# Optimization experiments

Hardware: AMD Instinct MI355X
Metric: run time of the kernel (lower is better)

## Reference

```python
import jax, jax.numpy as jnp
import numpy as np

D = 2048      # d_model
H = 16        # n_heads
M = 8         # n_modalities (== seq_len, forced by attn_mask shape)
S = 8         # seq_len per modality
E = 8         # num_experts
K = 3         # top_k
SPARSITY = 0.1


def setup_inputs() -> dict:
    key = jax.random.key(0)
    ks = jax.random.split(key, 24)
    w = lambda i, shape, s=0.02: (jax.random.normal(ks[i], shape, jnp.float32) * s)
    return {
        'feats': jax.random.normal(ks[0], (M, S, D), jnp.float32),
        'context': jax.random.normal(ks[1], (D,), jnp.float32),
        'mod_emb': jax.random.normal(ks[2], (M, D), jnp.float32),  # torch.randn
        'rW1': w(3, (D, 2 * D)), 'rb1': jnp.zeros((D,), jnp.float32),
        'rW2': w(4, (D // 2, D)), 'rb2': jnp.zeros((D // 2,), jnp.float32),
        'rW3': w(5, (1, D // 2)), 'rb3': jnp.zeros((1,), jnp.float32),
        'W_in': w(6, (3 * D, D)), 'b_in': jnp.zeros((3 * D,), jnp.float32),
        'W_out': w(7, (D, D)), 'b_out': jnp.zeros((D,), jnp.float32),
        'gW1': w(8, (D // 2, D)), 'gb1': jnp.zeros((D // 2,), jnp.float32),
        'gW2': w(9, (E, D // 2)), 'gb2': jnp.zeros((E,), jnp.float32),
        'eW1': w(10, (E, 2 * D, D)), 'eb1': jnp.zeros((E, 2 * D), jnp.float32),
        'eW2': w(11, (E, D, 2 * D)), 'eb2': jnp.zeros((E, D), jnp.float32),
        'e_gamma': jnp.ones((E, D), jnp.float32),
        'e_beta': jnp.zeros((E, D), jnp.float32),
    }


def reference(feats, context, mod_emb, rW1, rb1, rW2, rb2, rW3, rb3,
              W_in, b_in, W_out, b_out, gW1, gb1, gW2, gb2,
              eW1, eb1, eW2, eb2, e_gamma, e_beta):
    # --- modality embedding enhancement ---
    x = feats + mod_emb[:, None, :]                                # [M,S,D]

    # --- dynamic modality routing ---
    summ = x.mean(axis=1)                                          # [M,D] (mean over seq dim 0 of each 2D feat)
    comb = jnp.concatenate([summ, jnp.broadcast_to(context, summ.shape)], axis=-1)  # [M,2D]
    h = jax.nn.relu(comb @ rW1.T + rb1)
    h = jax.nn.relu(h @ rW2.T + rb2)
    rw = jax.nn.sigmoid(h @ rW3.T + rb3)[:, 0]                     # [M]
    rw = rw / rw.sum()                                             # sigmoid>0 so total>0 branch

    # --- sparse attention mask from routing weights ---
    wmat = rw[:, None] * rw[None, :]                               # [M,M]
    thr = jnp.quantile(wmat.reshape(-1), 1.0 - SPARSITY)
    mask = jnp.where(wmat < thr, jnp.float32(-1e9), jnp.float32(0.0))  # [M,M] == [S,S]

    # --- multi-head self-attention (batch=M modalities, seq=S, eval mode) ---
    qkv = x @ W_in.T + b_in                                        # [M,S,3D]
    q, k, v = jnp.split(qkv, 3, axis=-1)
    hd = D // H
    q = q.reshape(M, S, H, hd); k = k.reshape(M, S, H, hd); v = v.reshape(M, S, H, hd)
    scores = jnp.einsum('bqhd,bkhd->bhqk', q, k) / np.sqrt(hd)     # [M,H,S,S]
    scores = scores + mask                                         # broadcast [S,S] additive mask
    attn = jax.nn.softmax(scores, axis=-1)
    o = jnp.einsum('bhqk,bkhd->bqhd', attn, v).reshape(M, S, D)
    o = o @ W_out.T + b_out                                        # [M,S,D]

    # attended.mean(dim=0).squeeze() then view(-1)[:D] == first row of the mean
    attended = o.mean(axis=0)[0]                                   # [D]

    # --- mixture-of-experts fusion on the single token ---
    g = jax.nn.relu(attended @ gW1.T + gb1)
    gate_probs = jax.nn.softmax(g @ gW2.T + gb2)                   # [E]
    top_v, top_i = jax.lax.top_k(gate_probs, K)
    gates = jax.nn.softmax(top_v)                                  # renormalized top-k gates
    W1k, b1k = eW1[top_i], eb1[top_i]                              # [K,2D,D],[K,2D]
    W2k, b2k = eW2[top_i], eb2[top_i]                              # [K,D,2D],[K,D]
    gk, bk = e_gamma[top_i], e_beta[top_i]                         # [K,D]
    hh = jax.nn.gelu(jnp.einsum('d,kod->ko', attended, W1k) + b1k, approximate=False)
    y = jnp.einsum('ko,kdo->kd', hh, W2k) + b2k                    # [K,D]
    mu = y.mean(axis=-1, keepdims=True)
    var = ((y - mu) ** 2).mean(axis=-1, keepdims=True)
    ln = (y - mu) / jnp.sqrt(var + 1e-5) * gk + bk                 # per-expert LayerNorm
    fused = (gates[:, None] * ln).sum(axis=0)                      # [D]
    return fused, rw
```

## Files before the change

### kernel.cpp

```cpp
#include <hip/hip_runtime.h>
#include <math.h>

namespace {

constexpr int Dm = 2048;

using f4n = __attribute__((ext_vector_type(4))) float;

__device__ __forceinline__ float dot4(float4 u, float4 v) {
  return u.x * v.x + u.y * v.y + u.z * v.z + u.w * v.w;
}
__device__ __forceinline__ float4 add4(float4 u, float4 v) {
  return make_float4(u.x + v.x, u.y + v.y, u.z + v.z, u.w + v.w);
}
__device__ __forceinline__ float dot4nt(const float* p, float4 a) {
  f4n w = __builtin_nontemporal_load((const f4n*)p);
  return w.x * a.x + w.y * a.y + w.z * a.z + w.w * a.w;
}

__device__ __forceinline__ void top3_from_logits(const float* l, int* ti) {
  int used0 = -1, used1 = -1;
  for (int kk = 0; kk < 3; ++kk) {
    float bv = -1e30f; int bi = -1;
#pragma unroll
    for (int e = 0; e < 8; ++e) {
      if (e == used0 || e == used1) continue;
      if (l[e] > bv) { bv = l[e]; bi = e; }
    }
    ti[kk] = bi;
    if (kk == 0) used0 = bi; else if (kk == 1) used1 = bi;
  }
}

__global__ __launch_bounds__(256) void k_summ(const float* __restrict__ feats,
                                              const float* __restrict__ mod,
                                              float* __restrict__ summ,
                                              float* __restrict__ msum,
                                              float* __restrict__ logits) {
  int t4 = blockIdx.x * 256 + threadIdx.x;
  int elem = t4 * 4;
  int m = elem >> 11;
  float4 s = make_float4(0.f, 0.f, 0.f, 0.f);
#pragma unroll
  for (int t = 0; t < 8; ++t)
    s = add4(s, *(const float4*)(feats + ((size_t)(m * 8 + t) << 11) + (elem & 2047)));
  float4 md = *(const float4*)(mod + elem);
  *(float4*)(summ + elem) = make_float4(s.x * 0.125f + md.x, s.y * 0.125f + md.y,
                                        s.z * 0.125f + md.z, s.w * 0.125f + md.w);
  if (t4 < 512) {
    int i4 = t4 * 4;
    float4 acc = make_float4(0.f, 0.f, 0.f, 0.f);
#pragma unroll
    for (int mm = 0; mm < 8; ++mm)
      acc = add4(acc, *(const float4*)(mod + ((size_t)mm << 11) + i4));
    *(float4*)(msum + i4) = acc;
  }
  if (blockIdx.x == 0 && threadIdx.x < 8) logits[threadIdx.x] = 0.f;
}

__global__ __launch_bounds__(256) void k_big1(const float* __restrict__ summ,
                                              const float* __restrict__ ctx,
                                              const float* __restrict__ feats,
                                              const float* __restrict__ mod,
                                              const float* __restrict__ rW1,
                                              const float* __restrict__ rb1,
                                              const float* __restrict__ W_in,
                                              const float* __restrict__ b_in,
                                              float* __restrict__ h1,
                                              float* __restrict__ q0) {
  __shared__ float As[8 * Dm];
  int tid = threadIdx.x, wave = tid >> 6, lane = tid & 63;
  if (blockIdx.x < 512) {
    for (int t = tid; t < 8 * Dm; t += 256) As[t] = summ[t];
    __syncthreads();
    int j = blockIdx.x * 4 + wave;
    const float* Wr = rW1 + (size_t)j * 4096;
    float acc[8] = {0, 0, 0, 0, 0, 0, 0, 0};
    float accC = 0.f;
    for (int i = lane * 4; i < Dm; i += 256) {
      float4 w1 = *(const float4*)(Wr + i);
      float4 w2 = *(const float4*)(Wr + 2048 + i);
      float4 c = *(const float4*)(ctx + i);
      accC += dot4(w2, c);
#pragma unroll
      for (int m = 0; m < 8; ++m) {
        float4 a = *(const float4*)(As + (m << 11) + i);
        acc[m] += dot4(w1, a);
      }
    }
#pragma unroll
    for (int o = 32; o > 0; o >>= 1) {
      accC += __shfl_down(accC, o, 64);
#pragma unroll
      for (int m = 0; m < 8; ++m) acc[m] += __shfl_down(acc[m], o, 64);
    }
    if (lane == 0) {
      float base = accC + rb1[j];
#pragma unroll
      for (int m = 0; m < 8; ++m) h1[(m << 11) + j] = fmaxf(acc[m] + base, 0.f);
    }
  } else {
    for (int t = tid; t < 8 * Dm; t += 256) {
      int m = t >> 11, col = t & 2047;
      As[t] = feats[(size_t)(m * 8) * Dm + col] + mod[(m << 11) + col];
    }
    __syncthreads();
    int j = (blockIdx.x - 512) * 4 + wave;
    const float* Wr = W_in + (size_t)j * Dm;
    float acc[8] = {0, 0, 0, 0, 0, 0, 0, 0};
    for (int i = lane * 4; i < Dm; i += 256) {
      float4 w = *(const float4*)(Wr + i);
#pragma unroll
      for (int m = 0; m < 8; ++m) {
        float4 a = *(const float4*)(As + (m << 11) + i);
        acc[m] += dot4(w, a);
      }
    }
#pragma unroll
    for (int o = 32; o > 0; o >>= 1)
#pragma unroll
      for (int m = 0; m < 8; ++m) acc[m] += __shfl_down(acc[m], o, 64);
    if (lane == 0) {
      float b = b_in[j];
#pragma unroll
      for (int m = 0; m < 8; ++m) q0[(m << 11) + j] = acc[m] + b;
    }
  }
}

__global__ __launch_bounds__(256) void k_big2(const float* __restrict__ h1,
                                              const float* __restrict__ rW2,
                                              const float* __restrict__ rb2,
                                              const float* __restrict__ q0,
                                              const float* __restrict__ W_in,
                                              float* __restrict__ h2,
                                              float* __restrict__ qw) {
  __shared__ float As[8 * Dm];
  int tid = threadIdx.x, wave = tid >> 6, lane = tid & 63;
  if (blockIdx.x < 256) {
    for (int t = tid; t < 8 * Dm; t += 256) As[t] = h1[t];
    __syncthreads();
    int j = blockIdx.x * 4 + wave;
    const float* Wr = rW2 + (size_t)j * Dm;
    float acc[8] = {0, 0, 0, 0, 0, 0, 0, 0};
    for (int i = lane * 4; i < Dm; i += 256) {
      float4 w = *(const float4*)(Wr + i);
#pragma unroll
      for (int m = 0; m < 8; ++m) {
        float4 a = *(const float4*)(As + (m << 11) + i);
        acc[m] += dot4(w, a);
      }
    }
#pragma unroll
    for (int o = 32; o > 0; o >>= 1)
#pragma unroll
      for (int m = 0; m < 8; ++m) acc[m] += __shfl_down(acc[m], o, 64);
    if (lane == 0) {
      float b = rb2[j];
#pragma unroll
      for (int m = 0; m < 8; ++m) h2[m * 1024 + j] = fmaxf(acc[m] + b, 0.f);
    }
  } else {
    int bb = blockIdx.x - 256;
    int h = bb >> 3, chunk = bb & 7;
    int c0 = chunk * 256;
    float* qs = As;
    float* red = As + 1024;
    for (int t = tid; t < 1024; t += 256) {
      int m = t >> 7, d = t & 127;
      qs[t] = q0[(m << 11) + h * 128 + d];
    }
    __syncthreads();
    float4 acc[8];
#pragma unroll
    for (int m = 0; m < 8; ++m) acc[m] = make_float4(0.f, 0.f, 0.f, 0.f);
    const float* Wb = W_in + (size_t)(Dm + h * 128 + wave * 32) * Dm + c0 + lane * 4;
#pragma unroll 8
    for (int d = 0; d < 32; ++d) {
      float4 wv = *(const float4*)(Wb + (size_t)d * Dm);
#pragma unroll
      for (int m = 0; m < 8; ++m) {
        float q = qs[(m << 7) + wave * 32 + d];
        acc[m].x += wv.x * q; acc[m].y += wv.y * q;
        acc[m].z += wv.z * q; acc[m].w += wv.w * q;
      }
    }
#pragma unroll
    for (int m = 0; m < 8; ++m)
      *(float4*)(red + (((wave << 3) + m) << 8) + lane * 4) = acc[m];
    __syncthreads();
    int m = tid >> 5, c = (tid & 31) * 8;
    float4 s0 = make_float4(0.f, 0.f, 0.f, 0.f);
    float4 s1 = make_float4(0.f, 0.f, 0.f, 0.f);
#pragma unroll
    for (int w = 0; w < 4; ++w) {
      s0 = add4(s0, *(const float4*)(red + (((w << 3) + m) << 8) + c));
      s1 = add4(s1, *(const float4*)(red + (((w << 3) + m) << 8) + c + 4));
    }
    float* dst = qw + (size_t)(m * 16 + h) * Dm + c0 + c;
    *(float4*)dst = s0;
    *(float4*)(dst + 4) = s1;
  }
}

__global__ __launch_bounds__(256) void k_attnw(const float* __restrict__ h2,
                                               const float* __restrict__ rW3,
                                               const float* __restrict__ rb3,
                                               const float* __restrict__ qw,
                                               const float* __restrict__ feats,
                                               float* __restrict__ att,
                                               float* __restrict__ out_rw) {
  __shared__ float sig[8], wm[64], sv[64], mask_s[8];
  int tid = threadIdx.x, wave = tid >> 6, lane = tid & 63;
  for (int mi = 0; mi < 2; ++mi) {
    int m = wave + mi * 4;
    float acc = 0.f;
    for (int i = lane * 4; i < 1024; i += 256) {
      float4 w = *(const float4*)(rW3 + i);
      float4 a = *(const float4*)(h2 + m * 1024 + i);
      acc += dot4(w, a);
    }
#pragma unroll
    for (int o = 32; o > 0; o >>= 1) acc += __shfl_down(acc, o, 64);
    if (lane == 0) sig[m] = 1.f / (1.f + expf(-(acc + rb3[0])));
  }
  __syncthreads();
  if (tid < 64) {
    float tot = 0.f;
#pragma unroll
    for (int m = 0; m < 8; ++m) tot += sig[m];
    int r = tid >> 3, cc = tid & 7;
    wm[tid] = (sig[r] / tot) * (sig[cc] / tot);
    if (blockIdx.x == 0 && tid < 8) out_rw[tid] = sig[tid] / tot;
  }
  __syncthreads();
  if (tid < 64) {
    float v = wm[tid];
    int rank = 0;
    for (int t = 0; t < 64; ++t) {
      float u = wm[t];
      rank += (u < v) || (u == v && t < tid);
    }
    sv[rank] = v;
  }
  __syncthreads();
  if (tid < 8) {
    double pos = 0.9 * 63.0;
    int lo = (int)pos;
    double frac = pos - (double)lo;
    float thr = (float)((double)sv[lo] + frac * ((double)sv[lo + 1] - (double)sv[lo]));
    mask_s[tid] = (wm[tid] < thr) ? -1e9f : 0.f;
  }
  __syncthreads();
  {
    int mh = blockIdx.x * 4 + wave;
    int m = mh >> 4;
    const float* qr = qw + (size_t)mh * Dm;
    float sc[8];
#pragma unroll
    for (int k = 0; k < 8; ++k) {
      const float* fr = feats + (size_t)(m * 8 + k) * Dm;
      float acc = 0.f;
#pragma unroll
      for (int i = 0; i < 8; ++i) {
        int idx = lane * 4 + i * 256;
        acc += dot4(*(const float4*)(qr + idx), *(const float4*)(fr + idx));
      }
#pragma unroll
      for (int o = 32; o > 0; o >>= 1) acc += __shfl_xor(acc, o, 64);
      sc[k] = acc * 0.08838834764831845f + mask_s[k];
    }
    float mx = sc[0];
#pragma unroll
    for (int k = 1; k < 8; ++k) mx = fmaxf(mx, sc[k]);
    float se = 0.f;
#pragma unroll
    for (int k = 0; k < 8; ++k) { sc[k] = expf(sc[k] - mx); se += sc[k]; }
    float inv = 1.f / se;
    if (lane == 0) {
#pragma unroll
      for (int k = 0; k < 8; ++k) att[mh * 8 + k] = sc[k] * inv;
    }
  }
}

__global__ __launch_bounds__(256) void k_xbar(const float* __restrict__ att,
                                              const float* __restrict__ feats,
                                              const float* __restrict__ msum,
                                              float* __restrict__ xbar) {
  __shared__ float aw[64];
  int h = blockIdx.y;
  int i = blockIdx.x * 256 + threadIdx.x;
  if (threadIdx.x < 64) {
    int m = threadIdx.x >> 3, k = threadIdx.x & 7;
    aw[threadIdx.x] = att[(m * 16 + h) * 8 + k];
  }
  __syncthreads();
  float acc = msum[i];
#pragma unroll
  for (int b = 0; b < 64; ++b) acc += aw[b] * feats[(size_t)b * Dm + i];
  xbar[(size_t)h * Dm + i] = acc * 0.125f;
}

template <int ACT>
__global__ __launch_bounds__(256) void k_matvec8(const float* __restrict__ A, int G,
                                                 const float* __restrict__ W,
                                                 const float* __restrict__ b1,
                                                 float* __restrict__ out) {
  int j0 = blockIdx.x * 8;
  const float* Arow = A + (size_t)(j0 / G) * Dm;
  int wave = threadIdx.x >> 6, lane = threadIdx.x & 63;
  int j = j0 + wave * 2;
  const float* W0 = W + (size_t)j * Dm;
  const float* W1 = W0 + Dm;
  float acc0 = 0.f, acc1 = 0.f;
#pragma unroll 8
  for (int i = lane * 4; i < Dm; i += 256) {
    float4 a = *(const float4*)(Arow + i);
    acc0 += dot4(*(const float4*)(W0 + i), a);
    acc1 += dot4(*(const float4*)(W1 + i), a);
  }
#pragma unroll
  for (int o = 32; o > 0; o >>= 1) {
    acc0 += __shfl_down(acc0, o, 64);
    acc1 += __shfl_down(acc1, o, 64);
  }
  if (lane == 0) {
    float v0 = acc0 + b1[j], v1 = acc1 + b1[j + 1];
    if (ACT == 1) { v0 = fmaxf(v0, 0.f); v1 = fmaxf(v1, 0.f); }
    out[j] = v0;
    out[j + 1] = v1;
  }
}

__global__ __launch_bounds__(256) void k_gbufL(const float* __restrict__ attd,
                                               const float* __restrict__ gW1,
                                               const float* __restrict__ gb1,
                                               const float* __restrict__ gW2,
                                               float* __restrict__ logits) {
  __shared__ float gv[8];
  int tid = threadIdx.x, wave = tid >> 6, lane = tid & 63;
  int j0 = blockIdx.x * 8;
  int j = j0 + wave * 2;
  const float* W0 = gW1 + (size_t)j * Dm;
  const float* W1 = W0 + Dm;
  float acc0 = 0.f, acc1 = 0.f;
#pragma unroll 8
  for (int i = lane * 4; i < Dm; i += 256) {
    float4 a = *(const float4*)(attd + i);
    acc0 += dot4(*(const float4*)(W0 + i), a);
    acc1 += dot4(*(const float4*)(W1 + i), a);
  }
#pragma unroll
  for (int o = 32; o > 0; o >>= 1) {
    acc0 += __shfl_down(acc0, o, 64);
    acc1 += __shfl_down(acc1, o, 64);
  }
  if (lane == 0) {
    gv[wave * 2] = fmaxf(acc0 + gb1[j], 0.f);
    gv[wave * 2 + 1] = fmaxf(acc1 + gb1[j + 1], 0.f);
  }
  __syncthreads();
  if (tid < 8) {
    float pl = 0.f;
#pragma unroll
    for (int r = 0; r < 8; ++r) pl += gW2[tid * 1024 + j0 + r] * gv[r];
    atomicAdd(&logits[tid], pl);
  }
}

template <int IN, int ACT>
__global__ __launch_bounds__(256) void k_expert8(const float* __restrict__ A,
                                                 int a_stride_kk,
                                                 const float* __restrict__ Wbase,
                                                 size_t wstride,
                                                 const float* __restrict__ bbase,
                                                 int bstride,
                                                 const float* __restrict__ logits,
                                                 const float* __restrict__ gb2,
                                                 float* __restrict__ out, int OUT) {
  int kk = blockIdx.y;
  float l[8];
#pragma unroll
  for (int e = 0; e < 8; ++e) l[e] = logits[e] + gb2[e];
  int ti[3];
  top3_from_logits(l, ti);
  int ei = ti[kk];
  const float* Arow = A + (size_t)kk * a_stride_kk;
  int wave = threadIdx.x >> 6, lane = threadIdx.x & 63;
  int j = blockIdx.x * 8 + wave * 2;
  const float* W0 = Wbase + (size_t)ei * wstride + (size_t)j * IN;
  const float* W1 = W0 + IN;
  float acc0 = 0.f, acc1 = 0.f;
#pragma unroll 8
  for (int i = lane * 4; i < IN; i += 256) {
    float4 a = *(const float4*)(Arow + i);
    acc0 += dot4nt(W0 + i, a);
    acc1 += dot4nt(W1 + i, a);
  }
#pragma unroll
  for (int o = 32; o > 0; o >>= 1) {
    acc0 += __shfl_down(acc0, o, 64);
    acc1 += __shfl_down(acc1, o, 64);
  }
  if (lane == 0) {
    const float* bb = bbase + (size_t)ei * bstride;
    float v0 = acc0 + bb[j], v1 = acc1 + bb[j + 1];
    if (ACT == 2) {
      v0 = 0.5f * v0 * (1.f + erff(v0 * 0.70710678118654752f));
      v1 = 0.5f * v1 * (1.f + erff(v1 * 0.70710678118654752f));
    }
    out[(size_t)kk * OUT + j] = v0;
    out[(size_t)kk * OUT + j + 1] = v1;
  }
}

__global__ __launch_bounds__(256) void k_final(const float* __restrict__ y,
                                               const float* __restrict__ logits,
                                               const float* __restrict__ gb2,
                                               const float* __restrict__ e_gamma,
                                               const float* __restrict__ e_beta,
                                               float* __restrict__ outp) {
  __shared__ float ws_s[4], ws_ss[4];
  int tid = threadIdx.x, wave = tid >> 6, lane = tid & 63;
  float l[8];
#pragma unroll
  for (int e = 0; e < 8; ++e) l[e] = logits[e] + gb2[e];
  int ti[3];
  top3_from_logits(l, ti);
  float mx = l[0];
#pragma unroll
  for (int e = 1; e < 8; ++e) mx = fmaxf(mx, l[e]);
  float se = 0.f;
  float p[8];
#pragma unroll
  for (int e = 0; e < 8; ++e) { p[e] = expf(l[e] - mx); se += p[e]; }
  float tv0 = p[ti[0]] / se, tv1 = p[ti[1]] / se, tv2 = p[ti[2]] / se;
  float g0 = 1.f, g1 = expf(tv1 - tv0), g2 = expf(tv2 - tv0);
  float gs = g0 + g1 + g2;
  float gates[3] = {g0 / gs, g1 / gs, g2 / gs};
  float fused[8];
#pragma unroll
  for (int t = 0; t < 8; ++t) fused[t] = 0.f;
  for (int kk = 0; kk < 3; ++kk) {
    int ei = ti[kk];
    float gk = gates[kk];
    const float* yr = y + (size_t)kk * Dm;
    float s = 0.f, ss = 0.f;
    float vbuf[8];
#pragma unroll
    for (int t = 0; t < 8; ++t) {
      float v = yr[tid + 256 * t];
      vbuf[t] = v;
      s += v; ss += v * v;
    }
#pragma unroll
    for (int o = 32; o > 0; o >>= 1) {
      s += __shfl_down(s, o, 64);
      ss += __shfl_down(ss, o, 64);
    }
    if (lane == 0) { ws_s[wave] = s; ws_ss[wave] = ss; }
    __syncthreads();
    float S = ws_s[0] + ws_s[1] + ws_s[2] + ws_s[3];
    float SS = ws_ss[0] + ws_ss[1] + ws_ss[2] + ws_ss[3];
    float mu = S * (1.f / 2048.f);
    float var = SS * (1.f / 2048.f) - mu * mu;
    float rstd = rsqrtf(var + 1e-5f);
#pragma unroll
    for (int t = 0; t < 8; ++t) {
      int d = tid + 256 * t;
      fused[t] += gk * ((vbuf[t] - mu) * rstd * e_gamma[(size_t)ei * Dm + d] +
                        e_beta[(size_t)ei * Dm + d]);
    }
    __syncthreads();
  }
#pragma unroll
  for (int t = 0; t < 8; ++t) outp[tid + 256 * t] = fused[t];
}

}

extern "C" void kernel_launch(void* const* d_in, const int* in_sizes, int n_in,
                              void* d_out, int out_size, void* d_ws, size_t ws_size,
                              hipStream_t stream) {
  const float* feats   = (const float*)d_in[0];
  const float* context = (const float*)d_in[1];
  const float* mod_emb = (const float*)d_in[2];
  const float* rW1 = (const float*)d_in[3];
  const float* rb1 = (const float*)d_in[4];
  const float* rW2 = (const float*)d_in[5];
  const float* rb2 = (const float*)d_in[6];
  const float* rW3 = (const float*)d_in[7];
  const float* rb3 = (const float*)d_in[8];
  const float* W_in  = (const float*)d_in[9];
  const float* b_in  = (const float*)d_in[10];
  const float* W_out = (const float*)d_in[11];
  const float* b_out = (const float*)d_in[12];
  const float* gW1 = (const float*)d_in[13];
  const float* gb1 = (const float*)d_in[14];
  const float* gW2 = (const float*)d_in[15];
  const float* gb2 = (const float*)d_in[16];
  const float* eW1 = (const float*)d_in[17];
  const float* eb1 = (const float*)d_in[18];
  const float* eW2 = (const float*)d_in[19];
  const float* eb2 = (const float*)d_in[20];
  const float* e_gamma = (const float*)d_in[21];
  const float* e_beta  = (const float*)d_in[22];
  float* out = (float*)d_out;
  float* ws = (float*)d_ws;

  float* summ   = ws;
  float* msum   = summ + 16384;
  float* h1     = msum + 2048;
  float* h2     = h1 + 16384;
  float* q0     = h2 + 8192;
  float* qw     = q0 + 16384;
  float* att    = qw + 262144;
  float* xbar   = att + 1024;
  float* obar   = xbar + 32768;
  float* attd   = obar + 2048;
  float* logits = attd + 2048;
  float* hh     = logits + 8;
  float* ybuf   = hh + 12288;

  const int BIG = 1 << 30;

  hipLaunchKernelGGL(k_summ, dim3(16), dim3(256), 0, stream,
                     feats, mod_emb, summ, msum, logits);
  hipLaunchKernelGGL(k_big1, dim3(1024), dim3(256), 0, stream,
                     summ, context, feats, mod_emb, rW1, rb1, W_in, b_in, h1, q0);
  hipLaunchKernelGGL(k_big2, dim3(384), dim3(256), 0, stream,
                     h1, rW2, rb2, q0, W_in, h2, qw);
  hipLaunchKernelGGL(k_attnw, dim3(32), dim3(256), 0, stream,
                     h2, rW3, rb3, qw, feats, att, out + 2048);
  hipLaunchKernelGGL(k_xbar, dim3(8, 16), dim3(256), 0, stream, att, feats, msum, xbar);
  hipLaunchKernelGGL(k_matvec8<0>, dim3(256), dim3(256), 0, stream,
                     xbar, 128, W_in + (size_t)4096 * 2048, b_in + 4096, obar);
  hipLaunchKernelGGL(k_matvec8<0>, dim3(256), dim3(256), 0, stream,
                     obar, BIG, W_out, b_out, attd);
  hipLaunchKernelGGL(k_gbufL, dim3(128), dim3(256), 0, stream,
                     attd, gW1, gb1, gW2, logits);
  hipLaunchKernelGGL((k_expert8<2048, 2>), dim3(512, 3), dim3(256), 0, stream,
                     attd, 0, eW1, (size_t)4096 * 2048, eb1, 4096, logits, gb2, hh, 4096);
  hipLaunchKernelGGL((k_expert8<4096, 0>), dim3(256, 3), dim3(256), 0, stream,
                     hh, 4096, eW2, (size_t)2048 * 4096, eb2, 2048, logits, gb2, ybuf, 2048);
  hipLaunchKernelGGL(k_final, dim3(1), dim3(256), 0, stream,
                     ybuf, logits, gb2, e_gamma, e_beta, out);
}
```

Before: 116.9 us.

## Fuse attention-weight and xbar kernels into one per-head block; vectorize shared loads

Merges the attention-weight kernel and the xbar weighted-sum kernel into a single 16-block, 512-thread kernel. Each block handles one head, keeps the attention weights in shared memory and computes xbar directly, which removes one launch and the global att buffer. The shared-memory staging loops in the big GEMV kernels now use float4 loads instead of scalar loads. In exchange, each head block recomputes the routing sigmoid, and the xbar work now runs on only 16 blocks instead of 128, so parallelism in that stage drops.

```diff
diff --git a/kernel.cpp b/kernel.cpp
--- a/kernel.cpp
+++ b/kernel.cpp
@@ -71,7 +71,8 @@
   __shared__ float As[8 * Dm];
   int tid = threadIdx.x, wave = tid >> 6, lane = tid & 63;
   if (blockIdx.x < 512) {
-    for (int t = tid; t < 8 * Dm; t += 256) As[t] = summ[t];
+    for (int t4 = tid; t4 < 4096; t4 += 256)
+      ((float4*)As)[t4] = ((const float4*)summ)[t4];
     __syncthreads();
     int j = blockIdx.x * 4 + wave;
     const float* Wr = rW1 + (size_t)j * 4096;
@@ -100,9 +101,10 @@
       for (int m = 0; m < 8; ++m) h1[(m << 11) + j] = fmaxf(acc[m] + base, 0.f);
     }
   } else {
-    for (int t = tid; t < 8 * Dm; t += 256) {
-      int m = t >> 11, col = t & 2047;
-      As[t] = feats[(size_t)(m * 8) * Dm + col] + mod[(m << 11) + col];
+    for (int t4 = tid; t4 < 4096; t4 += 256) {
+      int m = t4 >> 9, col4 = t4 & 511;
+      ((float4*)As)[t4] = add4(((const float4*)(feats + (size_t)(m * 8) * Dm))[col4],
+                               ((const float4*)(mod + ((size_t)m << 11)))[col4]);
     }
     __syncthreads();
     int j = (blockIdx.x - 512) * 4 + wave;
@@ -138,7 +140,8 @@
   __shared__ float As[8 * Dm];
   int tid = threadIdx.x, wave = tid >> 6, lane = tid & 63;
   if (blockIdx.x < 256) {
-    for (int t = tid; t < 8 * Dm; t += 256) As[t] = h1[t];
+    for (int t4 = tid; t4 < 4096; t4 += 256)
+      ((float4*)As)[t4] = ((const float4*)h1)[t4];
     __syncthreads();
     int j = blockIdx.x * 4 + wave;
     const float* Wr = rW2 + (size_t)j * Dm;
@@ -166,9 +169,9 @@
     int c0 = chunk * 256;
     float* qs = As;
     float* red = As + 1024;
-    for (int t = tid; t < 1024; t += 256) {
-      int m = t >> 7, d = t & 127;
-      qs[t] = q0[(m << 11) + h * 128 + d];
+    for (int t4 = tid; t4 < 256; t4 += 256) {
+      int m = t4 >> 5, d4 = t4 & 31;
+      ((float4*)qs)[t4] = ((const float4*)(q0 + ((size_t)m << 11) + h * 128))[d4];
     }
     __syncthreads();
     float4 acc[8];
@@ -203,26 +206,29 @@
   }
 }
 
-__global__ __launch_bounds__(256) void k_attnw(const float* __restrict__ h2,
-                                               const float* __restrict__ rW3,
-                                               const float* __restrict__ rb3,
-                                               const float* __restrict__ qw,
-                                               const float* __restrict__ feats,
-                                               float* __restrict__ att,
-                                               float* __restrict__ out_rw) {
-  __shared__ float sig[8], wm[64], sv[64], mask_s[8];
+__global__ __launch_bounds__(512) void k_attn16(const float* __restrict__ h2,
+                                                const float* __restrict__ rW3,
+                                                const float* __restrict__ rb3,
+                                                const float* __restrict__ qw,
+                                                const float* __restrict__ feats,
+                                                const float* __restrict__ msum,
+                                                float* __restrict__ xbar,
+                                                float* __restrict__ out_rw) {
+  __shared__ float sig[8], wm[64], sv[64], mask_s[8], att[64];
   int tid = threadIdx.x, wave = tid >> 6, lane = tid & 63;
-  for (int mi = 0; mi < 2; ++mi) {
-    int m = wave + mi * 4;
+  int h = blockIdx.x;
+  {
     float acc = 0.f;
-    for (int i = lane * 4; i < 1024; i += 256) {
-      float4 w = *(const float4*)(rW3 + i);
-      float4 a = *(const float4*)(h2 + m * 1024 + i);
+#pragma unroll
+    for (int i = 0; i < 4; ++i) {
+      int idx = lane * 4 + i * 256;
+      float4 w = *(const float4*)(rW3 + idx);
+      float4 a = *(const float4*)(h2 + wave * 1024 + idx);
       acc += dot4(w, a);
     }
 #pragma unroll
     for (int o = 32; o > 0; o >>= 1) acc += __shfl_down(acc, o, 64);
-    if (lane == 0) sig[m] = 1.f / (1.f + expf(-(acc + rb3[0])));
+    if (lane == 0) sig[wave] = 1.f / (1.f + expf(-(acc + rb3[0])));
   }
   __syncthreads();
   if (tid < 64) {
@@ -231,7 +237,7 @@
     for (int m = 0; m < 8; ++m) tot += sig[m];
     int r = tid >> 3, cc = tid & 7;
     wm[tid] = (sig[r] / tot) * (sig[cc] / tot);
-    if (blockIdx.x == 0 && tid < 8) out_rw[tid] = sig[tid] / tot;
+    if (h == 0 && tid < 8) out_rw[tid] = sig[tid] / tot;
   }
   __syncthreads();
   if (tid < 64) {
@@ -253,9 +259,8 @@
   }
   __syncthreads();
   {
-    int mh = blockIdx.x * 4 + wave;
-    int m = mh >> 4;
-    const float* qr = qw + (size_t)mh * Dm;
+    int m = wave;
+    const float* qr = qw + (size_t)(m * 16 + h) * Dm;
     float sc[8];
 #pragma unroll
     for (int k = 0; k < 8; ++k) {
@@ -279,27 +284,22 @@
     float inv = 1.f / se;
     if (lane == 0) {
 #pragma unroll
-      for (int k = 0; k < 8; ++k) att[mh * 8 + k] = sc[k] * inv;
-    }
-  }
-}
-
-__global__ __launch_bounds__(256) void k_xbar(const float* __restrict__ att,
-                                              const float* __restrict__ feats,
-                                              const float* __restrict__ msum,
-                                              float* __restrict__ xbar) {
-  __shared__ float aw[64];
-  int h = blockIdx.y;
-  int i = blockIdx.x * 256 + threadIdx.x;
-  if (threadIdx.x < 64) {
-    int m = threadIdx.x >> 3, k = threadIdx.x & 7;
-    aw[threadIdx.x] = att[(m * 16 + h) * 8 + k];
+      for (int k = 0; k < 8; ++k) att[m * 8 + k] = sc[k] * inv;
+    }
   }
   __syncthreads();
-  float acc = msum[i];
-#pragma unroll
-  for (int b = 0; b < 64; ++b) acc += aw[b] * feats[(size_t)b * Dm + i];
-  xbar[(size_t)h * Dm + i] = acc * 0.125f;
+  {
+    int i4 = tid * 4;
+    float4 acc = *(const float4*)(msum + i4);
+#pragma unroll
+    for (int b = 0; b < 64; ++b) {
+      float a = att[b];
+      float4 f = *(const float4*)(feats + (size_t)b * Dm + i4);
+      acc.x += a * f.x; acc.y += a * f.y; acc.z += a * f.z; acc.w += a * f.w;
+    }
+    float4 r = make_float4(acc.x * 0.125f, acc.y * 0.125f, acc.z * 0.125f, acc.w * 0.125f);
+    *(float4*)(xbar + (size_t)h * Dm + i4) = r;
+  }
 }
 
 template <int ACT>
@@ -515,8 +515,7 @@
   float* h2     = h1 + 16384;
   float* q0     = h2 + 8192;
   float* qw     = q0 + 16384;
-  float* att    = qw + 262144;
-  float* xbar   = att + 1024;
+  float* xbar   = qw + 262144;
   float* obar   = xbar + 32768;
   float* attd   = obar + 2048;
   float* logits = attd + 2048;
@@ -531,9 +530,8 @@
                      summ, context, feats, mod_emb, rW1, rb1, W_in, b_in, h1, q0);
   hipLaunchKernelGGL(k_big2, dim3(384), dim3(256), 0, stream,
                      h1, rW2, rb2, q0, W_in, h2, qw);
-  hipLaunchKernelGGL(k_attnw, dim3(32), dim3(256), 0, stream,
-                     h2, rW3, rb3, qw, feats, att, out + 2048);
-  hipLaunchKernelGGL(k_xbar, dim3(8, 16), dim3(256), 0, stream, att, feats, msum, xbar);
+  hipLaunchKernelGGL(k_attn16, dim3(16), dim3(512), 0, stream,
+                     h2, rW3, rb3, qw, feats, msum, xbar, out + 2048);
   hipLaunchKernelGGL(k_matvec8<0>, dim3(256), dim3(256), 0, stream,
                      xbar, 128, W_in + (size_t)4096 * 2048, b_in + 4096, obar);
   hipLaunchKernelGGL(k_matvec8<0>, dim3(256), dim3(256), 0, stream,
```

New measurement: 118.8 us. About the same (+1.7%).
